# Performance work log

Hardware: AMD Instinct MI355X
Metric: run time of the kernel (lower is better)

The kernel has to match this reference:

```python
import jax, jax.numpy as jnp
import numpy as np

B, S, D, H = 2, 2048, 1024, 16
DK = D // H

def setup_inputs() -> dict:
    key = jax.random.key(0)
    ks = jax.random.split(key, 11)
    scale = 1.0 / np.sqrt(D)
    inp = {
        'query': jax.random.normal(ks[0], (B, S, D), jnp.float32),
        'key':   jax.random.normal(ks[1], (B, S, D), jnp.float32),
        'value': jax.random.normal(ks[2], (B, S, D), jnp.float32),
        'wq': jax.random.normal(ks[3], (D, D), jnp.float32) * scale,
        'bq': jax.random.normal(ks[4], (D,), jnp.float32) * 0.01,
        'wk': jax.random.normal(ks[5], (D, D), jnp.float32) * scale,
        'bk': jax.random.normal(ks[6], (D,), jnp.float32) * 0.01,
        'wv': jax.random.normal(ks[7], (D, D), jnp.float32) * scale,
        'bv': jax.random.normal(ks[8], (D,), jnp.float32) * 0.01,
        'wo': jax.random.normal(ks[9], (D, D), jnp.float32) * scale,
        'bo': jax.random.normal(ks[10], (D,), jnp.float32) * 0.01,
    }
    return inp

def reference(query, key, value, wq, bq, wk, bk, wv, bv, wo, bo):
    nb = query.shape[0]
    # projections: torch nn.Linear computes x @ W^T + b; here weights stored as (in,out)
    def proj(x, w, b):
        return (x @ w + b).reshape(nb, -1, H, DK).transpose(0, 2, 1, 3)  # [B,H,S,dk]
    q = proj(query, wq, bq)
    k = proj(key, wk, bk)
    v = proj(value, wv, bv)
    scores = jnp.einsum('bhqd,bhkd->bhqk', q, k) / jnp.sqrt(jnp.float32(DK))
    p = jax.nn.softmax(scores, axis=-1)  # dropout p=0 (eval)
    x = jnp.einsum('bhqk,bhkd->bhqd', p, v)
    x = x.transpose(0, 2, 1, 3).reshape(nb, -1, H * DK)
    return x @ wo + bo
```

## Files before the change

### kernel.cpp

```cpp
#include <hip/hip_runtime.h>


typedef __attribute__((ext_vector_type(8))) __bf16 bf16x8;
typedef __attribute__((ext_vector_type(4))) __bf16 bf16x4;
typedef __attribute__((ext_vector_type(8))) float f32x8;
typedef __attribute__((ext_vector_type(4))) float f32x4;

#define MFMA16 __builtin_amdgcn_mfma_f32_16x16x32_bf16

union Bf8 { bf16x8 v; __bf16 e[8]; };

__device__ inline f32x4 zero4() { f32x4 z; z[0]=z[1]=z[2]=z[3]=0.f; return z; }

__device__ inline float fast_exp2(float x) {
#if __has_builtin(__builtin_amdgcn_exp2f)
    return __builtin_amdgcn_exp2f(x);
#else
    return __expf(x * 0.6931471805599453f);
#endif
}

__device__ inline void load_lds16(const void* g, void* l) {
    __builtin_amdgcn_global_load_lds(
        (const __attribute__((address_space(1))) unsigned int*)g,
        (__attribute__((address_space(3))) unsigned int*)l, 16, 0, 0);
}

__global__ __launch_bounds__(256) void prep_all(
        const float* __restrict__ w0, const float* __restrict__ w1,
        const float* __restrict__ w2, const float* __restrict__ w3,
        const float* __restrict__ x0, const float* __restrict__ x1,
        const float* __restrict__ x2,
        __bf16* __restrict__ wt, __bf16* __restrict__ d0,
        __bf16* __restrict__ d1, __bf16* __restrict__ d2) {
    const int z = blockIdx.z, t = threadIdx.x;
    if (z < 4) {
        const float* src = z == 0 ? w0 : z == 1 ? w1 : z == 2 ? w2 : w3;
        __bf16* dst = wt + (size_t)z * 1048576;
        __shared__ float tile[32][33];
        const int tc = t & 31, tr = t >> 5;
        const int r0 = blockIdx.y * 32, c0 = blockIdx.x * 32;
#pragma unroll
        for (int i = 0; i < 4; i++) {
            int r = tr + i * 8;
            tile[r][tc] = src[(size_t)(r0 + r) * 1024 + c0 + tc];
        }
        __syncthreads();
#pragma unroll
        for (int i = 0; i < 4; i++) {
            int r = tr + i * 8;
            dst[(size_t)(c0 + r) * 1024 + r0 + tc] = (__bf16)tile[tc][r];
        }
    } else {
        const float* src = z == 4 ? x0 : z == 5 ? x1 : x2;
        __bf16* dst = z == 4 ? d0 : z == 5 ? d1 : d2;
        int bid = blockIdx.y * 32 + blockIdx.x;
        size_t g = ((size_t)bid * 256 + t) * 16;
#pragma unroll
        for (int h = 0; h < 2; h++) {
            f32x8 a = *(const f32x8*)&src[g + h * 8];
            Bf8 tmp;
#pragma unroll
            for (int j = 0; j < 8; j++) tmp.e[j] = (__bf16)a[j];
            *(bf16x8*)&dst[g + h * 8] = tmp.v;
        }
    }
}

template <int MODE, typename OutT>
__device__ inline void gemm_fast_core(__bf16* __restrict__ smem,
                                      const __bf16* __restrict__ A,
                                      const __bf16* __restrict__ Bt,
                                      const float* __restrict__ bias,
                                      OutT* __restrict__ out, float scale) {
    __bf16* As = smem;
    __bf16* Bs = smem + 8192;
    const int t = threadIdx.x;
    const int wave = t >> 6, lane = t & 63, lm = lane & 15, quad = lane >> 4;
    const int m0 = blockIdx.y * 128, n0 = blockIdx.x * 128;
    const int wm = (wave >> 1) * 64, wn = (wave & 1) * 64;

    f32x4 acc[4][4];
#pragma unroll
    for (int i = 0; i < 4; i++)
#pragma unroll
        for (int j = 0; j < 4; j++) acc[i][j] = zero4();

    for (int k0 = 0; k0 < 1024; k0 += 64) {
#pragma unroll
        for (int i = 0; i < 4; i++) {
            int s = i * 256 + t;
            int row = s >> 3, cb = (s & 7) ^ (row & 7);
            size_t goff = (size_t)row * 1024 + k0 + cb * 8;
            load_lds16(&A[(size_t)m0 * 1024 + goff],
                       &As[(size_t)(i * 256 + wave * 64) * 8]);
            load_lds16(&Bt[(size_t)n0 * 1024 + goff],
                       &Bs[(size_t)(i * 256 + wave * 64) * 8]);
        }
        __syncthreads();
#pragma unroll
        for (int ks = 0; ks < 2; ks++) {
            bf16x8 af[4], bfr[4];
#pragma unroll
            for (int mt = 0; mt < 4; mt++)
                af[mt] = *(const bf16x8*)&As[(wm + mt * 16 + lm) * 64 +
                                             (((ks * 4 + quad) ^ (lm & 7)) * 8)];
#pragma unroll
            for (int nt = 0; nt < 4; nt++)
                bfr[nt] = *(const bf16x8*)&Bs[(wn + nt * 16 + lm) * 64 +
                                              (((ks * 4 + quad) ^ (lm & 7)) * 8)];
#pragma unroll
            for (int mt = 0; mt < 4; mt++)
#pragma unroll
                for (int nt = 0; nt < 4; nt++)
                    acc[mt][nt] = MFMA16(af[mt], bfr[nt], acc[mt][nt], 0, 0, 0);
        }
        __syncthreads();
    }

    float bv4[4];
#pragma unroll
    for (int nt = 0; nt < 4; nt++) bv4[nt] = bias[n0 + wn + nt * 16 + lm];

    if (MODE == 2) {
#pragma unroll
        for (int mt = 0; mt < 4; mt++)
#pragma unroll
            for (int r = 0; r < 4; r++) {
                int rr = wm + mt * 16 + quad * 4 + r;
#pragma unroll
                for (int nt = 0; nt < 4; nt++) {
                    int c = wn + nt * 16 + lm;
                    smem[c * 128 + (rr ^ (8 * (c & 15)))] =
                        (__bf16)((acc[mt][nt][r] + bv4[nt]) * scale);
                }
            }
        __syncthreads();
        const int b = m0 >> 11;
#pragma unroll
        for (int it = 0; it < 8; it++) {
            int g = it * 256 + t;
            int c = g >> 4, gr = g & 15;
            bf16x8 v = *(const bf16x8*)&smem[c * 128 + ((gr * 8) ^ (8 * (c & 15)))];
            int col = n0 + c, hh = col >> 6, dk = col & 63;
            int sglob = (m0 & 2047) + gr * 8;
            size_t idx = (size_t)(b * 16 + hh) * 131072 + (size_t)dk * 2048 + sglob;
            *(bf16x8*)&out[idx] = v;
        }
    } else {
#pragma unroll
        for (int mt = 0; mt < 4; mt++) {
#pragma unroll
            for (int r = 0; r < 4; r++) {
                int row = m0 + wm + mt * 16 + quad * 4 + r;
#pragma unroll
                for (int nt = 0; nt < 4; nt++) {
                    int col = n0 + wn + nt * 16 + lm;
                    float val = (acc[mt][nt][r] + bv4[nt]) * scale;
                    size_t idx;
                    if (MODE == 0) {
                        idx = (size_t)row * 1024 + col;
                    } else {
                        int b = row >> 11, s = row & 2047, hh = col >> 6, dk = col & 63;
                        idx = (size_t)(b * 16 + hh) * 131072 + (size_t)s * 64 + dk;
                    }
                    out[idx] = (OutT)val;
                }
            }
        }
    }
}

__global__ __launch_bounds__(256) void proj_fast3(
        const __bf16* __restrict__ xq, const __bf16* __restrict__ xk,
        const __bf16* __restrict__ xv, const __bf16* __restrict__ WT,
        const float* __restrict__ bq, const float* __restrict__ bk,
        const float* __restrict__ bv,
        __bf16* __restrict__ Q, __bf16* __restrict__ K, __bf16* __restrict__ Vt) {
    __shared__ __bf16 smem[16384];
    int z = blockIdx.z;
    if (z == 0)
        gemm_fast_core<1, __bf16>(smem, xq, WT, bq, Q, 0.18033688f);
    else if (z == 1)
        gemm_fast_core<1, __bf16>(smem, xk, WT + 1048576, bk, K, 1.f);
    else
        gemm_fast_core<2, __bf16>(smem, xv, WT + 2097152, bv, Vt, 1.f);
}

__global__ __launch_bounds__(256) void out_proj_fast64(
        const __bf16* __restrict__ A, const __bf16* __restrict__ Bt,
        const float* __restrict__ bias, float* __restrict__ out) {
    __shared__ __bf16 As[8192];
    __shared__ __bf16 Bs[4096];
    const int t = threadIdx.x;
    const int wave = t >> 6, lane = t & 63, lm = lane & 15, quad = lane >> 4;
    const int m0 = blockIdx.y * 128, n0 = blockIdx.x * 64;
    const int wm = (wave >> 1) * 64, wn = (wave & 1) * 32;

    f32x4 acc[4][2];
#pragma unroll
    for (int i = 0; i < 4; i++) { acc[i][0] = zero4(); acc[i][1] = zero4(); }

    for (int k0 = 0; k0 < 1024; k0 += 64) {
#pragma unroll
        for (int i = 0; i < 4; i++) {
            int s = i * 256 + t;
            int row = s >> 3, cb = (s & 7) ^ (row & 7);
            load_lds16(&A[(size_t)(m0 + row) * 1024 + k0 + cb * 8],
                       &As[(size_t)(i * 256 + wave * 64) * 8]);
            if (i < 2)
                load_lds16(&Bt[(size_t)(n0 + row) * 1024 + k0 + cb * 8],
                           &Bs[(size_t)(i * 256 + wave * 64) * 8]);
        }
        __syncthreads();
#pragma unroll
        for (int ks = 0; ks < 2; ks++) {
            bf16x8 af[4], bfr[2];
#pragma unroll
            for (int mt = 0; mt < 4; mt++)
                af[mt] = *(const bf16x8*)&As[(wm + mt * 16 + lm) * 64 +
                                             (((ks * 4 + quad) ^ (lm & 7)) * 8)];
#pragma unroll
            for (int nt = 0; nt < 2; nt++)
                bfr[nt] = *(const bf16x8*)&Bs[(wn + nt * 16 + lm) * 64 +
                                              (((ks * 4 + quad) ^ (lm & 7)) * 8)];
#pragma unroll
            for (int mt = 0; mt < 4; mt++)
#pragma unroll
                for (int nt = 0; nt < 2; nt++)
                    acc[mt][nt] = MFMA16(af[mt], bfr[nt], acc[mt][nt], 0, 0, 0);
        }
        __syncthreads();
    }

    float bv2[2];
#pragma unroll
    for (int nt = 0; nt < 2; nt++) bv2[nt] = bias[n0 + wn + nt * 16 + lm];

#pragma unroll
    for (int mt = 0; mt < 4; mt++)
#pragma unroll
        for (int r = 0; r < 4; r++) {
            int row = m0 + wm + mt * 16 + quad * 4 + r;
#pragma unroll
            for (int nt = 0; nt < 2; nt++) {
                int col = n0 + wn + nt * 16 + lm;
                out[(size_t)row * 1024 + col] = acc[mt][nt][r] + bv2[nt];
            }
        }
}

__global__ __launch_bounds__(256, 2) void attn_kernel(
        const __bf16* __restrict__ Q, const __bf16* __restrict__ K,
        const __bf16* __restrict__ Vt, __bf16* __restrict__ O) {
    __shared__ __bf16 Ks[2][4096];
    __shared__ __bf16 Vs[2][4096];
    __shared__ __bf16 Ps[4 * 32 * 72];
    const int t = threadIdx.x;
    const int wave = t >> 6, lane = t & 63, lm = lane & 15, quad = lane >> 4;
    const int q0 = blockIdx.x * 128;
    const int bh = blockIdx.y;
    const size_t base = (size_t)bh * 131072;

    bf16x8 bq[2][2];
    {
        int qrow = q0 + wave * 32;
#pragma unroll
        for (int nt = 0; nt < 2; nt++)
#pragma unroll
            for (int ks = 0; ks < 2; ks++)
                bq[nt][ks] = *(const bf16x8*)
                    &Q[base + (size_t)(qrow + nt * 16 + lm) * 64 + ks * 32 + quad * 8];
    }

    float m_run[2], l_run[2];
#pragma unroll
    for (int n = 0; n < 2; n++) { m_run[n] = -1e30f; l_run[n] = 0.f; }
    f32x4 o_acc[4][2];
#pragma unroll
    for (int mt = 0; mt < 4; mt++)
#pragma unroll
        for (int n = 0; n < 2; n++) o_acc[mt][n] = zero4();

    __bf16* Pw = &Ps[wave * 32 * 72];

    auto stage = [&](int buf, int kv0) {
#pragma unroll
        for (int i = 0; i < 2; i++) {
            int s = i * 256 + t;
            int row = s >> 3, cb = (s & 7) ^ (row & 7);
            load_lds16(&K[base + (size_t)(kv0 + row) * 64 + cb * 8],
                       &Ks[buf][(i * 256 + wave * 64) * 8]);
            load_lds16(&Vt[base + (size_t)row * 2048 + kv0 + cb * 8],
                       &Vs[buf][(i * 256 + wave * 64) * 8]);
        }
    };

    stage(0, 0);
    __syncthreads();

    for (int it = 0; it < 32; ++it) {
        const int cur = it & 1;
        if (it < 31) stage(cur ^ 1, (it + 1) * 64);

        f32x4 sc[4][2];
        __builtin_amdgcn_s_setprio(1);
#pragma unroll
        for (int mt = 0; mt < 4; mt++) {
            sc[mt][0] = zero4();
            sc[mt][1] = zero4();
#pragma unroll
            for (int ks = 0; ks < 2; ks++) {
                bf16x8 ak = *(const bf16x8*)&Ks[cur][(mt * 16 + lm) * 64 +
                                                (((ks * 4 + quad) ^ (lm & 7)) * 8)];
                sc[mt][0] = MFMA16(ak, bq[0][ks], sc[mt][0], 0, 0, 0);
                sc[mt][1] = MFMA16(ak, bq[1][ks], sc[mt][1], 0, 0, 0);
            }
        }
        __builtin_amdgcn_s_setprio(0);

#pragma unroll
        for (int nt = 0; nt < 2; nt++) {
            float mx = -1e30f;
#pragma unroll
            for (int mt = 0; mt < 4; mt++)
#pragma unroll
                for (int r = 0; r < 4; r++) mx = fmaxf(mx, sc[mt][nt][r]);
            mx = fmaxf(mx, __shfl_xor(mx, 16));
            mx = fmaxf(mx, __shfl_xor(mx, 32));
            float mn = fmaxf(m_run[nt], mx);
            float alpha = fast_exp2(m_run[nt] - mn);
            m_run[nt] = mn;
            float su = 0.f;
#pragma unroll
            for (int mt = 0; mt < 4; mt++)
#pragma unroll
                for (int r = 0; r < 4; r++) {
                    float p = fast_exp2(sc[mt][nt][r] - mn);
                    sc[mt][nt][r] = p;
                    su += p;
                }
            su += __shfl_xor(su, 16);
            su += __shfl_xor(su, 32);
            l_run[nt] = l_run[nt] * alpha + su;
#pragma unroll
            for (int mt = 0; mt < 4; mt++)
#pragma unroll
                for (int r = 0; r < 4; r++) o_acc[mt][nt][r] *= alpha;
        }

#pragma unroll
        for (int nt = 0; nt < 2; nt++)
#pragma unroll
            for (int mt = 0; mt < 4; mt++) {
                bf16x4 pk;
#pragma unroll
                for (int r = 0; r < 4; r++) pk[r] = (__bf16)sc[mt][nt][r];
                *(bf16x4*)&Pw[(nt * 16 + lm) * 72 + mt * 16 + quad * 4] = pk;
            }
        __asm__ volatile("" ::: "memory");

        __builtin_amdgcn_s_setprio(1);
#pragma unroll
        for (int ks = 0; ks < 2; ks++) {
            bf16x8 bp[2];
#pragma unroll
            for (int nt = 0; nt < 2; nt++)
                bp[nt] = *(const bf16x8*)&Pw[(nt * 16 + lm) * 72 + ks * 32 + quad * 8];
#pragma unroll
            for (int mt = 0; mt < 4; mt++) {
                bf16x8 av = *(const bf16x8*)&Vs[cur][(mt * 16 + lm) * 64 +
                                                (((ks * 4 + quad) ^ (lm & 7)) * 8)];
                o_acc[mt][0] = MFMA16(av, bp[0], o_acc[mt][0], 0, 0, 0);
                o_acc[mt][1] = MFMA16(av, bp[1], o_acc[mt][1], 0, 0, 0);
            }
        }
        __builtin_amdgcn_s_setprio(0);

        __syncthreads();
    }

#pragma unroll
    for (int nt = 0; nt < 2; nt++) {
        float inv = 1.f / l_run[nt];
#pragma unroll
        for (int mt = 0; mt < 4; mt++) {
            bf16x4 pk;
#pragma unroll
            for (int r = 0; r < 4; r++) pk[r] = (__bf16)(o_acc[mt][nt][r] * inv);
            *(bf16x4*)&Pw[(nt * 16 + lm) * 72 + mt * 16 + quad * 4] = pk;
        }
    }
    __asm__ volatile("" ::: "memory");
    {
        const int b = bh >> 4, h = bh & 15;
        int ql = lane >> 1, half = lane & 1;
        int srow = q0 + wave * 32 + ql;
#pragma unroll
        for (int j = 0; j < 4; j++) {
            bf16x8 v = *(const bf16x8*)&Pw[ql * 72 + half * 32 + j * 8];
            *(bf16x8*)&O[(size_t)(b * 2048 + srow) * 1024 + h * 64 + half * 32 + j * 8] = v;
        }
    }
}

extern "C" void kernel_launch(void* const* d_in, const int* in_sizes, int n_in,
                              void* d_out, int out_size, void* d_ws, size_t ws_size,
                              hipStream_t stream) {
    if (ws_size < ((size_t)40 << 20)) return;

    const float* query = (const float*)d_in[0];
    const float* key_  = (const float*)d_in[1];
    const float* value = (const float*)d_in[2];
    const float* wq = (const float*)d_in[3];
    const float* bq = (const float*)d_in[4];
    const float* wk = (const float*)d_in[5];
    const float* bk = (const float*)d_in[6];
    const float* wv = (const float*)d_in[7];
    const float* bv = (const float*)d_in[8];
    const float* wo = (const float*)d_in[9];
    const float* bo = (const float*)d_in[10];
    float* out = (float*)d_out;

    char* ws = (char*)d_ws;
    __bf16* WT  = (__bf16*)(ws);
    __bf16* Qw  = (__bf16*)(ws + ((size_t)8  << 20));
    __bf16* Kw  = (__bf16*)(ws + ((size_t)16 << 20));
    __bf16* Vtw = (__bf16*)(ws + ((size_t)24 << 20));
    __bf16* Ow  = (__bf16*)(ws + ((size_t)32 << 20));

    __bf16* Xq = Ow;
    __bf16* Xk = (__bf16*)d_out;
    __bf16* Xv = (__bf16*)d_out + 4194304;

    prep_all<<<dim3(32, 32, 7), dim3(256), 0, stream>>>(
        wq, wk, wv, wo, query, key_, value, WT, Xq, Xk, Xv);
    proj_fast3<<<dim3(8, 32, 3), dim3(256), 0, stream>>>(
        Xq, Xk, Xv, WT, bq, bk, bv, Qw, Kw, Vtw);
    attn_kernel<<<dim3(16, 32), dim3(256), 0, stream>>>(Qw, Kw, Vtw, Ow);
    out_proj_fast64<<<dim3(16, 32), dim3(256), 0, stream>>>(
        Ow, WT + 3 * 1048576, bo, out);
}
```

Measured before the change: 240.8 us.

## Software-pipeline PV with next QK, lazy softmax rescale, permlane-swap reductions

Restructures the attention loop so each iteration does QK^T on the current K tile and P·V on the previous tile's P and V. K and V staging are split so V is loaded one iteration later, and one final PV step runs after the loop. Online-softmax rescaling of the accumulator is skipped when the new row max exceeds the running max by no more than 8 (exp2 domain). Row reductions use permlane16/32 swap instead of shuffles when those builtins are available. The aim is to overlap MFMA work with softmax and LDS traffic and to cut exp and multiply work, at the cost of more live registers and a wave-uniform branch.

```diff
diff --git a/kernel.cpp b/kernel.cpp
--- a/kernel.cpp
+++ b/kernel.cpp
@@ -5,6 +5,7 @@
 typedef __attribute__((ext_vector_type(4))) __bf16 bf16x4;
 typedef __attribute__((ext_vector_type(8))) float f32x8;
 typedef __attribute__((ext_vector_type(4))) float f32x4;
+typedef unsigned uv2 __attribute__((ext_vector_type(2)));
 
 #define MFMA16 __builtin_amdgcn_mfma_f32_16x16x32_bf16
 
@@ -17,6 +18,43 @@
     return __builtin_amdgcn_exp2f(x);
 #else
     return __expf(x * 0.6931471805599453f);
+#endif
+}
+
+#if __has_builtin(__builtin_amdgcn_permlane16_swap) && __has_builtin(__builtin_amdgcn_permlane32_swap)
+#define HAVE_PLSWAP 1
+#endif
+
+__device__ inline float red16_max(float x) {
+#ifdef HAVE_PLSWAP
+    uv2 r = __builtin_amdgcn_permlane16_swap(__float_as_uint(x), __float_as_uint(x), false, false);
+    return fmaxf(__uint_as_float(r[0]), __uint_as_float(r[1]));
+#else
+    return fmaxf(x, __shfl_xor(x, 16));
+#endif
+}
+__device__ inline float red32_max(float x) {
+#ifdef HAVE_PLSWAP
+    uv2 r = __builtin_amdgcn_permlane32_swap(__float_as_uint(x), __float_as_uint(x), false, false);
+    return fmaxf(__uint_as_float(r[0]), __uint_as_float(r[1]));
+#else
+    return fmaxf(x, __shfl_xor(x, 32));
+#endif
+}
+__device__ inline float red16_sum(float x) {
+#ifdef HAVE_PLSWAP
+    uv2 r = __builtin_amdgcn_permlane16_swap(__float_as_uint(x), __float_as_uint(x), false, false);
+    return __uint_as_float(r[0]) + __uint_as_float(r[1]);
+#else
+    return x + __shfl_xor(x, 16);
+#endif
+}
+__device__ inline float red32_sum(float x) {
+#ifdef HAVE_PLSWAP
+    uv2 r = __builtin_amdgcn_permlane32_swap(__float_as_uint(x), __float_as_uint(x), false, false);
+    return __uint_as_float(r[0]) + __uint_as_float(r[1]);
+#else
+    return x + __shfl_xor(x, 32);
 #endif
 }
 
@@ -284,24 +322,49 @@
 
     __bf16* Pw = &Ps[wave * 32 * 72];
 
-    auto stage = [&](int buf, int kv0) {
+    auto stageK = [&](int buf, int kv0) {
 #pragma unroll
         for (int i = 0; i < 2; i++) {
             int s = i * 256 + t;
             int row = s >> 3, cb = (s & 7) ^ (row & 7);
             load_lds16(&K[base + (size_t)(kv0 + row) * 64 + cb * 8],
                        &Ks[buf][(i * 256 + wave * 64) * 8]);
+        }
+    };
+    auto stageV = [&](int buf, int kv0) {
+#pragma unroll
+        for (int i = 0; i < 2; i++) {
+            int s = i * 256 + t;
+            int row = s >> 3, cb = (s & 7) ^ (row & 7);
             load_lds16(&Vt[base + (size_t)row * 2048 + kv0 + cb * 8],
                        &Vs[buf][(i * 256 + wave * 64) * 8]);
         }
     };
 
-    stage(0, 0);
+    auto pv_step = [&](int pbuf) {
+#pragma unroll
+        for (int ks = 0; ks < 2; ks++) {
+            bf16x8 bp[2];
+#pragma unroll
+            for (int nt = 0; nt < 2; nt++)
+                bp[nt] = *(const bf16x8*)&Pw[(nt * 16 + lm) * 72 + ks * 32 + quad * 8];
+#pragma unroll
+            for (int mt = 0; mt < 4; mt++) {
+                bf16x8 av = *(const bf16x8*)&Vs[pbuf][(mt * 16 + lm) * 64 +
+                                                (((ks * 4 + quad) ^ (lm & 7)) * 8)];
+                o_acc[mt][0] = MFMA16(av, bp[0], o_acc[mt][0], 0, 0, 0);
+                o_acc[mt][1] = MFMA16(av, bp[1], o_acc[mt][1], 0, 0, 0);
+            }
+        }
+    };
+
+    stageK(0, 0);
     __syncthreads();
 
     for (int it = 0; it < 32; ++it) {
         const int cur = it & 1;
-        if (it < 31) stage(cur ^ 1, (it + 1) * 64);
+        if (it < 31) stageK(cur ^ 1, (it + 1) * 64);
+        stageV(cur, it * 64);
 
         f32x4 sc[4][2];
         __builtin_amdgcn_s_setprio(1);
@@ -317,7 +380,9 @@
                 sc[mt][1] = MFMA16(ak, bq[1][ks], sc[mt][1], 0, 0, 0);
             }
         }
+        if (it > 0) pv_step(cur ^ 1);
         __builtin_amdgcn_s_setprio(0);
+        __asm__ volatile("" ::: "memory");
 
 #pragma unroll
         for (int nt = 0; nt < 2; nt++) {
@@ -326,27 +391,38 @@
             for (int mt = 0; mt < 4; mt++)
 #pragma unroll
                 for (int r = 0; r < 4; r++) mx = fmaxf(mx, sc[mt][nt][r]);
-            mx = fmaxf(mx, __shfl_xor(mx, 16));
-            mx = fmaxf(mx, __shfl_xor(mx, 32));
-            float mn = fmaxf(m_run[nt], mx);
-            float alpha = fast_exp2(m_run[nt] - mn);
-            m_run[nt] = mn;
-            float su = 0.f;
-#pragma unroll
-            for (int mt = 0; mt < 4; mt++)
-#pragma unroll
-                for (int r = 0; r < 4; r++) {
-                    float p = fast_exp2(sc[mt][nt][r] - mn);
-                    sc[mt][nt][r] = p;
-                    su += p;
-                }
-            su += __shfl_xor(su, 16);
-            su += __shfl_xor(su, 32);
-            l_run[nt] = l_run[nt] * alpha + su;
-#pragma unroll
-            for (int mt = 0; mt < 4; mt++)
-#pragma unroll
-                for (int r = 0; r < 4; r++) o_acc[mt][nt][r] *= alpha;
+            mx = red32_max(red16_max(mx));
+            float mo = m_run[nt];
+            if (__all(mx <= mo + 8.f)) {
+                float su = 0.f;
+#pragma unroll
+                for (int mt = 0; mt < 4; mt++)
+#pragma unroll
+                    for (int r = 0; r < 4; r++) {
+                        float p = fast_exp2(sc[mt][nt][r] - mo);
+                        sc[mt][nt][r] = p;
+                        su += p;
+                    }
+                l_run[nt] += red32_sum(red16_sum(su));
+            } else {
+                float mn = fmaxf(mo, mx);
+                float alpha = fast_exp2(mo - mn);
+                m_run[nt] = mn;
+                float su = 0.f;
+#pragma unroll
+                for (int mt = 0; mt < 4; mt++)
+#pragma unroll
+                    for (int r = 0; r < 4; r++) {
+                        float p = fast_exp2(sc[mt][nt][r] - mn);
+                        sc[mt][nt][r] = p;
+                        su += p;
+                    }
+                l_run[nt] = l_run[nt] * alpha + red32_sum(red16_sum(su));
+#pragma unroll
+                for (int mt = 0; mt < 4; mt++)
+#pragma unroll
+                    for (int r = 0; r < 4; r++) o_acc[mt][nt][r] *= alpha;
+            }
         }
 
 #pragma unroll
@@ -360,25 +436,12 @@
             }
         __asm__ volatile("" ::: "memory");
 
-        __builtin_amdgcn_s_setprio(1);
-#pragma unroll
-        for (int ks = 0; ks < 2; ks++) {
-            bf16x8 bp[2];
-#pragma unroll
-            for (int nt = 0; nt < 2; nt++)
-                bp[nt] = *(const bf16x8*)&Pw[(nt * 16 + lm) * 72 + ks * 32 + quad * 8];
-#pragma unroll
-            for (int mt = 0; mt < 4; mt++) {
-                bf16x8 av = *(const bf16x8*)&Vs[cur][(mt * 16 + lm) * 64 +
-                                                (((ks * 4 + quad) ^ (lm & 7)) * 8)];
-                o_acc[mt][0] = MFMA16(av, bp[0], o_acc[mt][0], 0, 0, 0);
-                o_acc[mt][1] = MFMA16(av, bp[1], o_acc[mt][1], 0, 0, 0);
-            }
-        }
-        __builtin_amdgcn_s_setprio(0);
-
-        __syncthreads();
-    }
+        __syncthreads();
+    }
+
+    __builtin_amdgcn_s_setprio(1);
+    pv_step(1);
+    __builtin_amdgcn_s_setprio(0);
 
 #pragma unroll
     for (int nt = 0; nt < 2; nt++) {
@@ -392,6 +455,7 @@
         }
     }
     __asm__ volatile("" ::: "memory");
+    __syncthreads();
     {
         const int b = bh >> 4, h = bh & 15;
         int ql = lane >> 1, half = lane & 1;
```

New measurement: 234.1 us. -2.8%, faster.
